# Performance work log

Measured on AMD Instinct MI355X. Metric: run time of the kernel, lower is better.

Reference implementation:

```python
import jax, jax.numpy as jnp
import numpy as np

EPS = 1e-12  # torch F.normalize eps

def _l2norm(v, axis):
    n = jnp.linalg.norm(v, axis=axis, keepdims=True)
    return v / jnp.maximum(n, EPS)

def setup_inputs() -> dict:
    key = jax.random.key(0)
    k1, k2, k3 = jax.random.split(key, 3)
    N, D, H, W, K = 32, 512, 40, 40, 64
    x = jax.random.normal(k1, (N, D, H, W), dtype=jnp.float32)
    conv_weight = jax.random.normal(k2, (K, D), dtype=jnp.float32) * 0.05
    centroids = jax.random.uniform(k3, (K, D), dtype=jnp.float32)
    return {"x": x, "conv_weight": conv_weight, "centroids": centroids}

def reference(x, conv_weight, centroids):
    N, D, H, W = x.shape
    K = centroids.shape[0]
    # descriptor-wise L2 normalization over channel dim
    x = _l2norm(x, axis=1)
    x_flat = x.reshape(N, D, H * W)                       # [N, D, S]
    # 1x1 conv == per-pixel linear: [K,D] @ [N,D,S] -> [N,K,S]
    logits = jnp.einsum('kd,nds->nks', conv_weight, x_flat)
    soft_assign = jax.nn.softmax(logits, axis=1)          # softmax over clusters
    # vlad[n,k,d] = sum_s a[n,k,s] * (x[n,d,s] - c[k,d])
    #            = (a @ x^T) - (sum_s a) * c   -- two GEMM-like ops, no K-loop
    agg = jnp.einsum('nks,nds->nkd', soft_assign, x_flat)  # [N, K, D]
    a_sum = soft_assign.sum(axis=2)                        # [N, K]
    vlad = agg - a_sum[:, :, None] * centroids[None, :, :]
    # intra-normalization over D, flatten, global L2 normalization
    vlad = _l2norm(vlad, axis=2)
    vlad = vlad.reshape(N, K * D)
    vlad = _l2norm(vlad, axis=1)
    return vlad
```

## Files before the change

kernel.cpp:

```cpp
#include <hip/hip_runtime.h>
#include <math.h>

#define N_ 32
#define D_ 512
#define S_ 1600
#define K_ 64

typedef __attribute__((ext_vector_type(8))) short short8;
typedef __attribute__((ext_vector_type(4))) float f32x4;

static __device__ __forceinline__ short f2bf(float f) {
    unsigned u = __float_as_uint(f);
    u += 0x7fffu + ((u >> 16) & 1u);
    return (short)(u >> 16);
}

__global__ __launch_bounds__(256) void kW(const float* __restrict__ w,
                                          short* __restrict__ w16)
{
    int i4 = (blockIdx.x * 256 + threadIdx.x) * 4;
    float4 v = *(const float4*)&w[i4];
    short4 h = {f2bf(v.x), f2bf(v.y), f2bf(v.z), f2bf(v.w)};
    *(short4*)&w16[i4] = h;
}

__global__ __launch_bounds__(256) void kX(const float* __restrict__ x,
                                          short* __restrict__ x16,
                                          float* __restrict__ inv)
{
    __shared__ float pssq[4][64];
    const int tid = threadIdx.x;
    const int n  = blockIdx.x / 25;
    const int s0 = (blockIdx.x % 25) * 64;
    const int sx = tid & 63;
    const int dg = tid >> 6;

    const float* xb = x + (size_t)n * D_ * S_ + s0 + sx;
    short* ob = x16 + (size_t)n * D_ * S_ + s0 + sx;

    float ss = 0.f;
#pragma unroll 8
    for (int r = dg; r < D_; r += 4) {
        float v = xb[(size_t)r * S_];
        ss += v * v;
        ob[(size_t)r * S_] = f2bf(v);
    }
    pssq[dg][sx] = ss;
    __syncthreads();
    if (tid < 64) {
        float t = pssq[0][tid] + pssq[1][tid] + pssq[2][tid] + pssq[3][tid];
        inv[(size_t)n * S_ + s0 + tid] = 1.0f / fmaxf(sqrtf(t), 1e-12f);
    }
}

__global__ __launch_bounds__(256) void kA(const short* __restrict__ x16,
                                          const short* __restrict__ w16,
                                          const float* __restrict__ inv,
                                          short* __restrict__ aprime,
                                          float* __restrict__ asum)
{
    __shared__ short T[32 * 68];
    __shared__ float wred[2][4][32];

    const int tid = threadIdx.x;
    const int n  = blockIdx.x / 50;
    const int s0 = (blockIdx.x % 50) * 32;
    const int wv = tid >> 6;
    const int l  = tid & 63;
    const int lk = l & 15;
    const int q  = l >> 4;
    const int s2 = (tid & 15) * 2;
    const int rr = tid >> 4;

    const short* xb = x16 + (size_t)n * D_ * S_ + s0;

    f32x4 acc[2];
    acc[0] = (f32x4){0.f, 0.f, 0.f, 0.f};
    acc[1] = (f32x4){0.f, 0.f, 0.f, 0.f};

    for (int dc = 0; dc < D_; dc += 64) {
        __syncthreads();
#pragma unroll
        for (int j = 0; j < 4; ++j) {
            const int row = rr + 16 * j;
            unsigned pv = *(const unsigned*)&xb[(size_t)(dc + row) * S_ + s2];
            T[s2 * 68 + row]       = (short)(pv & 0xffffu);
            T[(s2 + 1) * 68 + row] = (short)(pv >> 16);
        }
        __syncthreads();

#pragma unroll
        for (int kst = 0; kst < 2; ++kst) {
            short8 af = *(const short8*)&w16[(16 * wv + lk) * D_ + dc + kst * 32 + q * 8];
#pragma unroll
            for (int st = 0; st < 2; ++st) {
                const short* bp = &T[(st * 16 + lk) * 68 + kst * 32 + q * 8];
                short4 b0 = *(const short4*)bp;
                short4 b1 = *(const short4*)(bp + 4);
                short8 bf = {b0.x, b0.y, b0.z, b0.w, b1.x, b1.y, b1.z, b1.w};
                acc[st] = __builtin_amdgcn_mfma_f32_16x16x32_bf16(af, bf, acc[st], 0, 0, 0);
            }
        }
    }

    float lg[2][4], invv[2];
#pragma unroll
    for (int st = 0; st < 2; ++st) {
        invv[st] = inv[(size_t)n * S_ + s0 + st * 16 + lk];
#pragma unroll
        for (int r = 0; r < 4; ++r) lg[st][r] = acc[st][r] * invv[st];
    }
#pragma unroll
    for (int st = 0; st < 2; ++st) {
        float m = fmaxf(fmaxf(lg[st][0], lg[st][1]), fmaxf(lg[st][2], lg[st][3]));
        m = fmaxf(m, __shfl_xor(m, 16));
        m = fmaxf(m, __shfl_xor(m, 32));
        if (q == 0) wred[0][wv][st * 16 + lk] = m;
    }
    __syncthreads();
    float gm[2];
#pragma unroll
    for (int st = 0; st < 2; ++st) {
        float m = wred[0][0][st * 16 + lk];
        m = fmaxf(m, wred[0][1][st * 16 + lk]);
        m = fmaxf(m, wred[0][2][st * 16 + lk]);
        m = fmaxf(m, wred[0][3][st * 16 + lk]);
        gm[st] = m;
    }
    float e[2][4];
#pragma unroll
    for (int st = 0; st < 2; ++st) {
        float s = 0.f;
#pragma unroll
        for (int r = 0; r < 4; ++r) {
            e[st][r] = __expf(lg[st][r] - gm[st]);
            s += e[st][r];
        }
        s += __shfl_xor(s, 16);
        s += __shfl_xor(s, 32);
        if (q == 0) wred[1][wv][st * 16 + lk] = s;
    }
    __syncthreads();
    float rs[2];
#pragma unroll
    for (int st = 0; st < 2; ++st) {
        float s = wred[1][0][st * 16 + lk] + wred[1][1][st * 16 + lk]
                + wred[1][2][st * 16 + lk] + wred[1][3][st * 16 + lk];
        rs[st] = 1.0f / s;
    }

    short* apb = aprime + (size_t)n * K_ * S_ + s0;
#pragma unroll
    for (int r = 0; r < 4; ++r) {
        const int k = 16 * wv + 4 * q + r;
        float accp = 0.f;
#pragma unroll
        for (int st = 0; st < 2; ++st) {
            float p = e[st][r] * rs[st];
            apb[(size_t)k * S_ + st * 16 + lk] = f2bf(p * invv[st]);
            accp += p;
        }
        accp += __shfl_xor(accp, 1);
        accp += __shfl_xor(accp, 2);
        accp += __shfl_xor(accp, 4);
        accp += __shfl_xor(accp, 8);
        if (lk == 0) atomicAdd(&asum[n * K_ + k], accp);
    }
}

__global__ __launch_bounds__(256) void kB(const short* __restrict__ x16,
                                          const short* __restrict__ aprime,
                                          float* __restrict__ aggp)
{
    const int bid = blockIdx.x;
    const int n  = bid / 40;
    const int dt = (bid % 40) / 10;
    const int sp = bid % 10;
    const int wv = threadIdx.x >> 6;
    const int l  = threadIdx.x & 63;
    const int lk = l & 15;
    const int q  = l >> 4;
    const int dbase = dt * 128 + wv * 32;

    const short* ap = aprime + (size_t)n * K_ * S_;
    const short* xb = x16 + (size_t)n * D_ * S_;

    f32x4 acc[4][2];
#pragma unroll
    for (int kt = 0; kt < 4; ++kt)
#pragma unroll
        for (int ds = 0; ds < 2; ++ds) acc[kt][ds] = (f32x4){0.f, 0.f, 0.f, 0.f};

#pragma unroll
    for (int kst = 0; kst < 5; ++kst) {
        const int s = sp * 160 + kst * 32 + q * 8;
        short8 af[4];
#pragma unroll
        for (int kt = 0; kt < 4; ++kt)
            af[kt] = *(const short8*)&ap[(size_t)(kt * 16 + lk) * S_ + s];
        short8 bf[2];
#pragma unroll
        for (int ds = 0; ds < 2; ++ds)
            bf[ds] = *(const short8*)&xb[(size_t)(dbase + ds * 16 + lk) * S_ + s];
#pragma unroll
        for (int kt = 0; kt < 4; ++kt)
#pragma unroll
            for (int ds = 0; ds < 2; ++ds)
                acc[kt][ds] = __builtin_amdgcn_mfma_f32_16x16x32_bf16(af[kt], bf[ds], acc[kt][ds], 0, 0, 0);
    }

    float* ab = aggp + ((size_t)sp * N_ + n) * K_ * D_;
#pragma unroll
    for (int kt = 0; kt < 4; ++kt)
#pragma unroll
        for (int ds = 0; ds < 2; ++ds)
#pragma unroll
            for (int r = 0; r < 4; ++r)
                ab[(size_t)(kt * 16 + 4 * q + r) * D_ + dbase + ds * 16 + lk] = acc[kt][ds][r];
}

__global__ __launch_bounds__(256) void kC(const float* __restrict__ aggp,
                                          const float* __restrict__ asum,
                                          const float* __restrict__ cent,
                                          float* __restrict__ out)
{
    __shared__ float red[4];
    const int tid = threadIdx.x;
    const int nk = blockIdx.x;
    const int k = nk & 63;
    const float as = asum[nk];
    const float* cb = cent + (size_t)k * D_;

    float v0 = 0.f, v1 = 0.f;
#pragma unroll
    for (int p = 0; p < 10; ++p) {
        const float* ag = aggp + (size_t)p * N_ * K_ * D_ + (size_t)nk * D_;
        v0 += ag[tid];
        v1 += ag[tid + 256];
    }
    v0 -= as * cb[tid];
    v1 -= as * cb[tid + 256];
    float ssq = v0 * v0 + v1 * v1;

    ssq += __shfl_xor(ssq, 32);
    ssq += __shfl_xor(ssq, 16);
    ssq += __shfl_xor(ssq, 8);
    ssq += __shfl_xor(ssq, 4);
    ssq += __shfl_xor(ssq, 2);
    ssq += __shfl_xor(ssq, 1);
    if ((tid & 63) == 0) red[tid >> 6] = ssq;
    __syncthreads();
    const float total = red[0] + red[1] + red[2] + red[3];
    const float scale = 1.0f / (fmaxf(sqrtf(total), 1e-12f) * 8.0f);

    out[(size_t)nk * D_ + tid]       = v0 * scale;
    out[(size_t)nk * D_ + tid + 256] = v1 * scale;
}

extern "C" void kernel_launch(void* const* d_in, const int* in_sizes, int n_in,
                              void* d_out, int out_size, void* d_ws, size_t ws_size,
                              hipStream_t stream)
{
    const float* x    = (const float*)d_in[0];
    const float* w    = (const float*)d_in[1];
    const float* cent = (const float*)d_in[2];
    float* out = (float*)d_out;

    float* aggp   = (float*)d_ws;
    float* asum   = aggp + (size_t)10 * N_ * K_ * D_;
    float* invb   = asum + (size_t)N_ * K_;
    short* aprime = (short*)(invb + (size_t)N_ * S_);
    short* w16    = aprime + (size_t)N_ * K_ * S_;
    short* x16    = w16 + (size_t)K_ * D_;

    hipMemsetAsync(asum, 0, (size_t)N_ * K_ * sizeof(float), stream);

    kW<<<32, 256, 0, stream>>>(w, w16);
    kX<<<N_ * (S_ / 64), 256, 0, stream>>>(x, x16, invb);
    kA<<<N_ * (S_ / 32), 256, 0, stream>>>(x16, w16, invb, aprime, asum);
    kB<<<N_ * 4 * 10, 256, 0, stream>>>(x16, aprime, aggp);
    kC<<<N_ * K_, 256, 0, stream>>>(aggp, asum, cent, out);
}
```

Before: 227.4 us.

## Fuse soft-assignment and aggregation GEMMs into one kernel, drop atomics

Merges kA (logits and softmax) and kB (assignment times x aggregation) into a single kernel kAB. The bf16 assignment tile now stays in LDS instead of going through global memory, and per-split assignment sums are written to a partial buffer that kC reduces, which removes the atomics and the memset. Each block recomputes the full logits GEMM for its 160-pixel chunk, and this is done twice, once per D-half (dq). Only 640 blocks are launched and each holds a large LDS tile (about 33KB), so occupancy and parallelism may suffer.

```diff
diff --git a/kernel.cpp b/kernel.cpp
--- a/kernel.cpp
+++ b/kernel.cpp
@@ -5,6 +5,9 @@
 #define D_ 512
 #define S_ 1600
 #define K_ 64
+#define SP_ 10
+#define PD_ 520
+#define PA_ 40
 
 typedef __attribute__((ext_vector_type(8))) short short8;
 typedef __attribute__((ext_vector_type(4))) float f32x4;
@@ -53,188 +56,177 @@
     }
 }
 
-__global__ __launch_bounds__(256) void kA(const short* __restrict__ x16,
-                                          const short* __restrict__ w16,
-                                          const float* __restrict__ inv,
-                                          short* __restrict__ aprime,
-                                          float* __restrict__ asum)
-{
-    __shared__ short T[32 * 68];
+__global__ __launch_bounds__(256) void kAB(const short* __restrict__ x16,
+                                           const short* __restrict__ w16,
+                                           const float* __restrict__ inv,
+                                           float* __restrict__ aggp,
+                                           float* __restrict__ asump)
+{
+    __shared__ short T[32 * PD_];
+    __shared__ short AL[64 * PA_];
     __shared__ float wred[2][4][32];
 
     const int tid = threadIdx.x;
-    const int n  = blockIdx.x / 50;
-    const int s0 = (blockIdx.x % 50) * 32;
+    const int bid = blockIdx.x;
+    const int n  = bid / 20;
+    const int rm = bid % 20;
+    const int sp = rm >> 1;
+    const int dq = rm & 1;
     const int wv = tid >> 6;
     const int l  = tid & 63;
     const int lk = l & 15;
     const int q  = l >> 4;
+    const int sbase = sp * 160;
+    const int dwave = dq * 256 + wv * 64;
+
+    const short* xn = x16 + (size_t)n * D_ * S_;
     const int s2 = (tid & 15) * 2;
-    const int rr = tid >> 4;
-
-    const short* xb = x16 + (size_t)n * D_ * S_ + s0;
-
-    f32x4 acc[2];
-    acc[0] = (f32x4){0.f, 0.f, 0.f, 0.f};
-    acc[1] = (f32x4){0.f, 0.f, 0.f, 0.f};
-
-    for (int dc = 0; dc < D_; dc += 64) {
-        __syncthreads();
-#pragma unroll
-        for (int j = 0; j < 4; ++j) {
-            const int row = rr + 16 * j;
-            unsigned pv = *(const unsigned*)&xb[(size_t)(dc + row) * S_ + s2];
-            T[s2 * 68 + row]       = (short)(pv & 0xffffu);
-            T[(s2 + 1) * 68 + row] = (short)(pv >> 16);
-        }
-        __syncthreads();
-
-#pragma unroll
-        for (int kst = 0; kst < 2; ++kst) {
-            short8 af = *(const short8*)&w16[(16 * wv + lk) * D_ + dc + kst * 32 + q * 8];
+    const int r0 = tid >> 4;
+
+    f32x4 agg[4][4];
+#pragma unroll
+    for (int kt = 0; kt < 4; ++kt)
+#pragma unroll
+        for (int ds = 0; ds < 4; ++ds) agg[kt][ds] = (f32x4){0.f, 0.f, 0.f, 0.f};
+    float sreg[2][4] = {{0.f,0.f,0.f,0.f},{0.f,0.f,0.f,0.f}};
+
+    for (int c = 0; c < 5; ++c) {
+        const int sc = sbase + c * 32;
+        __syncthreads();
+#pragma unroll 8
+        for (int j = 0; j < 32; ++j) {
+            const int row = r0 + 16 * j;
+            unsigned pv = *(const unsigned*)&xn[(size_t)row * S_ + sc + s2];
+            T[s2 * PD_ + row]       = (short)(pv & 0xffffu);
+            T[(s2 + 1) * PD_ + row] = (short)(pv >> 16);
+        }
+        __syncthreads();
+
+        f32x4 lacc[2];
+        lacc[0] = (f32x4){0.f, 0.f, 0.f, 0.f};
+        lacc[1] = (f32x4){0.f, 0.f, 0.f, 0.f};
+#pragma unroll
+        for (int dstep = 0; dstep < 16; ++dstep) {
+            short8 af = *(const short8*)&w16[(16 * wv + lk) * D_ + dstep * 32 + q * 8];
 #pragma unroll
             for (int st = 0; st < 2; ++st) {
-                const short* bp = &T[(st * 16 + lk) * 68 + kst * 32 + q * 8];
-                short4 b0 = *(const short4*)bp;
-                short4 b1 = *(const short4*)(bp + 4);
-                short8 bf = {b0.x, b0.y, b0.z, b0.w, b1.x, b1.y, b1.z, b1.w};
-                acc[st] = __builtin_amdgcn_mfma_f32_16x16x32_bf16(af, bf, acc[st], 0, 0, 0);
+                short8 bfr = *(const short8*)&T[(st * 16 + lk) * PD_ + dstep * 32 + q * 8];
+                lacc[st] = __builtin_amdgcn_mfma_f32_16x16x32_bf16(af, bfr, lacc[st], 0, 0, 0);
             }
         }
-    }
-
-    float lg[2][4], invv[2];
-#pragma unroll
-    for (int st = 0; st < 2; ++st) {
-        invv[st] = inv[(size_t)n * S_ + s0 + st * 16 + lk];
-#pragma unroll
-        for (int r = 0; r < 4; ++r) lg[st][r] = acc[st][r] * invv[st];
-    }
-#pragma unroll
-    for (int st = 0; st < 2; ++st) {
-        float m = fmaxf(fmaxf(lg[st][0], lg[st][1]), fmaxf(lg[st][2], lg[st][3]));
-        m = fmaxf(m, __shfl_xor(m, 16));
-        m = fmaxf(m, __shfl_xor(m, 32));
-        if (q == 0) wred[0][wv][st * 16 + lk] = m;
-    }
-    __syncthreads();
-    float gm[2];
-#pragma unroll
-    for (int st = 0; st < 2; ++st) {
-        float m = wred[0][0][st * 16 + lk];
-        m = fmaxf(m, wred[0][1][st * 16 + lk]);
-        m = fmaxf(m, wred[0][2][st * 16 + lk]);
-        m = fmaxf(m, wred[0][3][st * 16 + lk]);
-        gm[st] = m;
-    }
-    float e[2][4];
-#pragma unroll
-    for (int st = 0; st < 2; ++st) {
-        float s = 0.f;
-#pragma unroll
-        for (int r = 0; r < 4; ++r) {
-            e[st][r] = __expf(lg[st][r] - gm[st]);
-            s += e[st][r];
-        }
-        s += __shfl_xor(s, 16);
-        s += __shfl_xor(s, 32);
-        if (q == 0) wred[1][wv][st * 16 + lk] = s;
-    }
-    __syncthreads();
-    float rs[2];
-#pragma unroll
-    for (int st = 0; st < 2; ++st) {
-        float s = wred[1][0][st * 16 + lk] + wred[1][1][st * 16 + lk]
-                + wred[1][2][st * 16 + lk] + wred[1][3][st * 16 + lk];
-        rs[st] = 1.0f / s;
-    }
-
-    short* apb = aprime + (size_t)n * K_ * S_ + s0;
+
+        float lg[2][4], invv[2];
+#pragma unroll
+        for (int st = 0; st < 2; ++st) {
+            invv[st] = inv[(size_t)n * S_ + sc + st * 16 + lk];
+#pragma unroll
+            for (int r = 0; r < 4; ++r) lg[st][r] = lacc[st][r] * invv[st];
+        }
+#pragma unroll
+        for (int st = 0; st < 2; ++st) {
+            float m = fmaxf(fmaxf(lg[st][0], lg[st][1]), fmaxf(lg[st][2], lg[st][3]));
+            m = fmaxf(m, __shfl_xor(m, 16));
+            m = fmaxf(m, __shfl_xor(m, 32));
+            if (q == 0) wred[0][wv][st * 16 + lk] = m;
+        }
+        __syncthreads();
+        float gm[2];
+#pragma unroll
+        for (int st = 0; st < 2; ++st) {
+            float m = wred[0][0][st * 16 + lk];
+            m = fmaxf(m, wred[0][1][st * 16 + lk]);
+            m = fmaxf(m, wred[0][2][st * 16 + lk]);
+            m = fmaxf(m, wred[0][3][st * 16 + lk]);
+            gm[st] = m;
+        }
+        float e[2][4];
+#pragma unroll
+        for (int st = 0; st < 2; ++st) {
+            float s = 0.f;
+#pragma unroll
+            for (int r = 0; r < 4; ++r) {
+                e[st][r] = __expf(lg[st][r] - gm[st]);
+                s += e[st][r];
+            }
+            s += __shfl_xor(s, 16);
+            s += __shfl_xor(s, 32);
+            if (q == 0) wred[1][wv][st * 16 + lk] = s;
+        }
+        __syncthreads();
+#pragma unroll
+        for (int st = 0; st < 2; ++st) {
+            float s = wred[1][0][st * 16 + lk] + wred[1][1][st * 16 + lk]
+                    + wred[1][2][st * 16 + lk] + wred[1][3][st * 16 + lk];
+            float rs = 1.0f / s;
+#pragma unroll
+            for (int r = 0; r < 4; ++r) {
+                float p = e[st][r] * rs;
+                sreg[st][r] += p;
+                AL[(16 * wv + 4 * q + r) * PA_ + st * 16 + lk] = f2bf(p * invv[st]);
+            }
+        }
+        __syncthreads();
+
+        short8 aal[4], bfx[4];
+#pragma unroll
+        for (int kt = 0; kt < 4; ++kt)
+            aal[kt] = *(const short8*)&AL[(kt * 16 + lk) * PA_ + q * 8];
+#pragma unroll
+        for (int ds = 0; ds < 4; ++ds)
+            bfx[ds] = *(const short8*)&xn[(size_t)(dwave + ds * 16 + lk) * S_ + sc + q * 8];
+#pragma unroll
+        for (int kt = 0; kt < 4; ++kt)
+#pragma unroll
+            for (int ds = 0; ds < 4; ++ds)
+                agg[kt][ds] = __builtin_amdgcn_mfma_f32_16x16x32_bf16(aal[kt], bfx[ds], agg[kt][ds], 0, 0, 0);
+    }
+
+    float* ab = aggp + ((size_t)sp * N_ + n) * K_ * D_;
+#pragma unroll
+    for (int kt = 0; kt < 4; ++kt)
+#pragma unroll
+        for (int ds = 0; ds < 4; ++ds)
+#pragma unroll
+            for (int r = 0; r < 4; ++r)
+                ab[(size_t)(kt * 16 + 4 * q + r) * D_ + dwave + ds * 16 + lk] = agg[kt][ds][r];
+
+    float t4[4];
 #pragma unroll
     for (int r = 0; r < 4; ++r) {
-        const int k = 16 * wv + 4 * q + r;
-        float accp = 0.f;
-#pragma unroll
-        for (int st = 0; st < 2; ++st) {
-            float p = e[st][r] * rs[st];
-            apb[(size_t)k * S_ + st * 16 + lk] = f2bf(p * invv[st]);
-            accp += p;
-        }
-        accp += __shfl_xor(accp, 1);
-        accp += __shfl_xor(accp, 2);
-        accp += __shfl_xor(accp, 4);
-        accp += __shfl_xor(accp, 8);
-        if (lk == 0) atomicAdd(&asum[n * K_ + k], accp);
-    }
-}
-
-__global__ __launch_bounds__(256) void kB(const short* __restrict__ x16,
-                                          const short* __restrict__ aprime,
-                                          float* __restrict__ aggp)
-{
-    const int bid = blockIdx.x;
-    const int n  = bid / 40;
-    const int dt = (bid % 40) / 10;
-    const int sp = bid % 10;
-    const int wv = threadIdx.x >> 6;
-    const int l  = threadIdx.x & 63;
-    const int lk = l & 15;
-    const int q  = l >> 4;
-    const int dbase = dt * 128 + wv * 32;
-
-    const short* ap = aprime + (size_t)n * K_ * S_;
-    const short* xb = x16 + (size_t)n * D_ * S_;
-
-    f32x4 acc[4][2];
-#pragma unroll
-    for (int kt = 0; kt < 4; ++kt)
-#pragma unroll
-        for (int ds = 0; ds < 2; ++ds) acc[kt][ds] = (f32x4){0.f, 0.f, 0.f, 0.f};
-
-#pragma unroll
-    for (int kst = 0; kst < 5; ++kst) {
-        const int s = sp * 160 + kst * 32 + q * 8;
-        short8 af[4];
-#pragma unroll
-        for (int kt = 0; kt < 4; ++kt)
-            af[kt] = *(const short8*)&ap[(size_t)(kt * 16 + lk) * S_ + s];
-        short8 bf[2];
-#pragma unroll
-        for (int ds = 0; ds < 2; ++ds)
-            bf[ds] = *(const short8*)&xb[(size_t)(dbase + ds * 16 + lk) * S_ + s];
-#pragma unroll
-        for (int kt = 0; kt < 4; ++kt)
-#pragma unroll
-            for (int ds = 0; ds < 2; ++ds)
-                acc[kt][ds] = __builtin_amdgcn_mfma_f32_16x16x32_bf16(af[kt], bf[ds], acc[kt][ds], 0, 0, 0);
-    }
-
-    float* ab = aggp + ((size_t)sp * N_ + n) * K_ * D_;
-#pragma unroll
-    for (int kt = 0; kt < 4; ++kt)
-#pragma unroll
-        for (int ds = 0; ds < 2; ++ds)
-#pragma unroll
-            for (int r = 0; r < 4; ++r)
-                ab[(size_t)(kt * 16 + 4 * q + r) * D_ + dbase + ds * 16 + lk] = acc[kt][ds][r];
+        float t = sreg[0][r] + sreg[1][r];
+        t += __shfl_xor(t, 1);
+        t += __shfl_xor(t, 2);
+        t += __shfl_xor(t, 4);
+        t += __shfl_xor(t, 8);
+        t4[r] = t;
+    }
+    if (lk == 0 && dq == 0) {
+        float4 st4 = {t4[0], t4[1], t4[2], t4[3]};
+        *(float4*)&asump[((size_t)sp * N_ + n) * K_ + 16 * wv + 4 * q] = st4;
+    }
 }
 
 __global__ __launch_bounds__(256) void kC(const float* __restrict__ aggp,
-                                          const float* __restrict__ asum,
+                                          const float* __restrict__ asump,
                                           const float* __restrict__ cent,
                                           float* __restrict__ out)
 {
     __shared__ float red[4];
     const int tid = threadIdx.x;
     const int nk = blockIdx.x;
+    const int n = nk >> 6;
     const int k = nk & 63;
-    const float as = asum[nk];
+
+    float as = 0.f;
+#pragma unroll
+    for (int p = 0; p < SP_; ++p)
+        as += asump[((size_t)p * N_ + n) * K_ + k];
+
     const float* cb = cent + (size_t)k * D_;
-
     float v0 = 0.f, v1 = 0.f;
 #pragma unroll
-    for (int p = 0; p < 10; ++p) {
-        const float* ag = aggp + (size_t)p * N_ * K_ * D_ + (size_t)nk * D_;
+    for (int p = 0; p < SP_; ++p) {
+        const float* ag = aggp + ((size_t)p * N_ + n) * K_ * D_ + (size_t)k * D_;
         v0 += ag[tid];
         v1 += ag[tid + 256];
     }
@@ -266,18 +258,14 @@
     const float* cent = (const float*)d_in[2];
     float* out = (float*)d_out;
 
-    float* aggp   = (float*)d_ws;
-    float* asum   = aggp + (size_t)10 * N_ * K_ * D_;
-    float* invb   = asum + (size_t)N_ * K_;
-    short* aprime = (short*)(invb + (size_t)N_ * S_);
-    short* w16    = aprime + (size_t)N_ * K_ * S_;
-    short* x16    = w16 + (size_t)K_ * D_;
-
-    hipMemsetAsync(asum, 0, (size_t)N_ * K_ * sizeof(float), stream);
+    float* aggp  = (float*)d_ws;
+    float* asump = aggp + (size_t)SP_ * N_ * K_ * D_;
+    float* invb  = asump + (size_t)SP_ * N_ * K_;
+    short* w16   = (short*)(invb + (size_t)N_ * S_);
+    short* x16   = w16 + (size_t)K_ * D_;
 
     kW<<<32, 256, 0, stream>>>(w, w16);
     kX<<<N_ * (S_ / 64), 256, 0, stream>>>(x, x16, invb);
-    kA<<<N_ * (S_ / 32), 256, 0, stream>>>(x16, w16, invb, aprime, asum);
-    kB<<<N_ * 4 * 10, 256, 0, stream>>>(x16, aprime, aggp);
-    kC<<<N_ * K_, 256, 0, stream>>>(aggp, asum, cent, out);
-}
+    kAB<<<N_ * SP_ * 2, 256, 0, stream>>>(x16, w16, invb, aggp, asump);
+    kC<<<N_ * K_, 256, 0, stream>>>(aggp, asump, cent, out);
+}
```

Result: no change. 224.7 us (-1.2%).
